# Performance work log

Measured on AMD Instinct MI355X. Metric: run time of the kernel, lower is better.

Reference implementation:

```python
import jax, jax.numpy as jnp
import numpy as np

ALPHA = 0.001  # plasticity learning rate from the source module
B, I, H = 64, 512, 1024
D = I + H


def _xavier(k, shape):
    fan_out, fan_in = shape
    lim = float(np.sqrt(6.0 / (fan_in + fan_out)))
    return jax.random.uniform(k, shape, minval=-lim, maxval=lim, dtype=jnp.float32)


def setup_inputs() -> dict:
    key = jax.random.key(0)
    ks = jax.random.split(key, 9)
    inputs = jax.random.normal(ks[0], (B, I), dtype=jnp.float32)
    hidden = 0.1 * jax.random.normal(ks[1], (B, H), dtype=jnp.float32)
    # per-sample plastic fast weights (nonzero to exercise the matvec path)
    wih = 0.01 * jax.random.normal(ks[2], (B, H, D), dtype=jnp.float32)
    Wih_a = _xavier(ks[3], (H, D))
    Wih_b = _xavier(ks[4], (H, D))
    Wih_c = _xavier(ks[5], (H, D))
    Wih_d = _xavier(ks[6], (H, D))
    bih = jnp.zeros((H,), dtype=jnp.float32)
    W_dop = _xavier(ks[7], (H, D))
    b_dop = jnp.zeros((H,), dtype=jnp.float32)
    return {"inputs": inputs, "hidden": hidden, "wih": wih,
            "Wih_a": Wih_a, "Wih_b": Wih_b, "Wih_c": Wih_c, "Wih_d": Wih_d,
            "bih": bih, "W_dop": W_dop, "b_dop": b_dop}


def reference(inputs, hidden, wih, Wih_a, Wih_b, Wih_c, Wih_d, bih, W_dop, b_dop):
    # x = cat(inputs, hidden): [B, D]
    x = jnp.concatenate([inputs, hidden], axis=1)
    # dopamine_signal is computed in the source but never used downstream;
    # kept here for fidelity (XLA will DCE it).
    _dopamine = jax.nn.sigmoid(x @ W_dop.T + b_dop)  # noqa: F841
    # batched matvec over the plastic fast weights: [B,H]
    new_hidden = jnp.tanh(jnp.einsum('bj,bkj->bk', x, wih) + bih)
    y = new_hidden[:, :, None]   # [B, H, 1]
    xb = x[:, None, :]           # [B, 1, D]
    # Hebbian outer-product update (the two 'ones' bmms are just broadcasts)
    wih_new = wih + ALPHA * (y * xb * Wih_a + xb * Wih_b + y * Wih_c + Wih_d)
    return new_hidden, wih_new
```

## Files before the change

kernel.cpp:

```cpp
#include <hip/hip_runtime.h>

constexpr int Bn = 64;
constexpr int In = 512;
constexpr int Hn = 1024;
constexpr int Dn = 1536;
constexpr float ALPHA = 0.001f;

typedef float nfloat4 __attribute__((ext_vector_type(4)));

__global__ __launch_bounds__(256) void prnn_fused_kernel(
    const float* __restrict__ inputs,
    const float* __restrict__ hidden,
    const float* __restrict__ wih,
    const float* __restrict__ Wa,
    const float* __restrict__ Wb,
    const float* __restrict__ Wc,
    const float* __restrict__ Wd,
    const float* __restrict__ bih,
    float* __restrict__ out_hidden,
    float* __restrict__ out_wih)
{
    __shared__ nfloat4 sW[4 * (Dn / 4)];

    const int k   = blockIdx.x;
    const int tid = threadIdx.x;

    {
        const nfloat4* wa4 = (const nfloat4*)(Wa + (size_t)k * Dn);
        const nfloat4* wb4 = (const nfloat4*)(Wb + (size_t)k * Dn);
        const nfloat4* wc4 = (const nfloat4*)(Wc + (size_t)k * Dn);
        const nfloat4* wd4 = (const nfloat4*)(Wd + (size_t)k * Dn);
        #pragma unroll
        for (int e = 0; e < 2; ++e) {
            const int i = tid + e * 256;
            if (i < 384) {
                sW[i]        = wa4[i] * ALPHA;
                sW[384 + i]  = wb4[i] * ALPHA;
                sW[768 + i]  = wc4[i] * ALPHA;
                sW[1152 + i] = wd4[i] * ALPHA;
            }
        }
    }
    __syncthreads();

    const int wave = tid >> 6;
    const int lane = tid & 63;
    const int b0   = wave * 16;
    const float bk = bih[k];
    const int base = lane * 4;

    nfloat4 w[4][6];
    nfloat4 xb[2][6];

    auto load_x = [&](int b, nfloat4 (&x)[6]) {
        const float* __restrict__ xin  = inputs + b * In;
        const float* __restrict__ xhid = hidden + b * Hn;
        #pragma unroll
        for (int c = 0; c < 6; ++c) {
            const int idx = c * 256 + base;
            x[c] = (c < 2) ? *(const nfloat4*)(xin + idx)
                           : *(const nfloat4*)(xhid + (idx - In));
        }
    };

    #pragma unroll
    for (int g = 0; g < 4; ++g) {
        const int bg = b0 + g * 4;

        #pragma unroll
        for (int q = 0; q < 4; ++q) {
            const float* __restrict__ wrow =
                wih + ((size_t)(bg + q) * Hn + k) * Dn;
            #pragma unroll
            for (int c = 0; c < 6; ++c)
                w[q][c] = *(const nfloat4*)(wrow + c * 256 + base);
        }
        load_x(bg, xb[0]);

        #pragma unroll
        for (int q = 0; q < 4; ++q) {
            if (q < 3) load_x(bg + q + 1, xb[(q + 1) & 1]);
            nfloat4 (&x)[6] = xb[q & 1];

            float acc = 0.0f;
            #pragma unroll
            for (int c = 0; c < 6; ++c) {
                nfloat4 p = w[q][c] * x[c];
                acc += (p.x + p.y) + (p.z + p.w);
            }
            #pragma unroll
            for (int off = 32; off > 0; off >>= 1)
                acc += __shfl_xor(acc, off, 64);

            const float y = tanhf(acc + bk);
            const int b = bg + q;
            if (lane == 0) out_hidden[b * Hn + k] = y;

            float* __restrict__ orow = out_wih + ((size_t)b * Hn + k) * Dn;
            #pragma unroll
            for (int c = 0; c < 6; ++c) {
                const int e = c * 64 + lane;
                const nfloat4 m1 = x[c] * sW[e]       + sW[768 + e];
                const nfloat4 m2 = x[c] * sW[384 + e] + sW[1152 + e];
                const nfloat4 o  = (w[q][c] + m2) + y * m1;
                __builtin_nontemporal_store(o, (nfloat4*)(orow + c * 256 + base));
            }
        }
    }
}

extern "C" void kernel_launch(void* const* d_in, const int* in_sizes, int n_in,
                              void* d_out, int out_size, void* d_ws, size_t ws_size,
                              hipStream_t stream) {
    const float* inputs = (const float*)d_in[0];
    const float* hidden = (const float*)d_in[1];
    const float* wih    = (const float*)d_in[2];
    const float* Wa     = (const float*)d_in[3];
    const float* Wb     = (const float*)d_in[4];
    const float* Wc     = (const float*)d_in[5];
    const float* Wd     = (const float*)d_in[6];
    const float* bih    = (const float*)d_in[7];

    float* out_hidden = (float*)d_out;
    float* out_wih    = (float*)d_out + (size_t)Bn * Hn;

    prnn_fused_kernel<<<dim3(Hn), dim3(256), 0, stream>>>(
        inputs, hidden, wih, Wa, Wb, Wc, Wd, bih, out_hidden, out_wih);
}
```

Before: 164.3 us.

## Remap blocks to (batch, 64-row k tile) and stream shared weights from L2

The work split changes from one block per hidden row k (covering all batches) to one block per (batch, 64-row chunk of k). Each wave handles 16 rows and keeps its x vector in registers for the whole block. The LDS staging of the four Wa..Wd rows is removed; those rows are now read straight from global memory for every (b,k), relying on L2/LLC reuse across the 64 batch blocks. The wih row loads are double-buffered so the next row is in flight during the current compute. In exchange, global read traffic for the shared weights rises unless the cache absorbs it.

```diff
diff --git a/kernel.cpp b/kernel.cpp
--- a/kernel.cpp
+++ b/kernel.cpp
@@ -20,91 +20,83 @@
     float* __restrict__ out_hidden,
     float* __restrict__ out_wih)
 {
-    __shared__ nfloat4 sW[4 * (Dn / 4)];
-
-    const int k   = blockIdx.x;
-    const int tid = threadIdx.x;
-
-    {
-        const nfloat4* wa4 = (const nfloat4*)(Wa + (size_t)k * Dn);
-        const nfloat4* wb4 = (const nfloat4*)(Wb + (size_t)k * Dn);
-        const nfloat4* wc4 = (const nfloat4*)(Wc + (size_t)k * Dn);
-        const nfloat4* wd4 = (const nfloat4*)(Wd + (size_t)k * Dn);
-        #pragma unroll
-        for (int e = 0; e < 2; ++e) {
-            const int i = tid + e * 256;
-            if (i < 384) {
-                sW[i]        = wa4[i] * ALPHA;
-                sW[384 + i]  = wb4[i] * ALPHA;
-                sW[768 + i]  = wc4[i] * ALPHA;
-                sW[1152 + i] = wd4[i] * ALPHA;
-            }
-        }
-    }
-    __syncthreads();
-
-    const int wave = tid >> 6;
-    const int lane = tid & 63;
-    const int b0   = wave * 16;
-    const float bk = bih[k];
+    const int bid  = blockIdx.x;
+    const int k0   = (bid & 15) << 6;
+    const int b    = bid >> 4;
+    const int wv   = threadIdx.x >> 6;
+    const int lane = threadIdx.x & 63;
     const int base = lane * 4;
 
-    nfloat4 w[4][6];
-    nfloat4 xb[2][6];
-
-    auto load_x = [&](int b, nfloat4 (&x)[6]) {
-        const float* __restrict__ xin  = inputs + b * In;
-        const float* __restrict__ xhid = hidden + b * Hn;
+    nfloat4 x[6];
+    {
+        const float* __restrict__ xin = inputs + b * In;
+        const float* __restrict__ xh  = hidden + b * Hn;
         #pragma unroll
         for (int c = 0; c < 6; ++c) {
             const int idx = c * 256 + base;
             x[c] = (c < 2) ? *(const nfloat4*)(xin + idx)
-                           : *(const nfloat4*)(xhid + (idx - In));
+                           : *(const nfloat4*)(xh + (idx - In));
         }
+    }
+
+    nfloat4 wb2[2][6];
+
+    auto wrow_ptr = [&](int i) {
+        const int k = k0 + wv + (i << 2);
+        return wih + ((size_t)b * Hn + k) * Dn;
     };
 
+    {
+        const float* __restrict__ p = wrow_ptr(0);
+        #pragma unroll
+        for (int c = 0; c < 6; ++c)
+            wb2[0][c] = *(const nfloat4*)(p + c * 256 + base);
+    }
+
     #pragma unroll
-    for (int g = 0; g < 4; ++g) {
-        const int bg = b0 + g * 4;
+    for (int i = 0; i < 16; ++i) {
+        const int k = k0 + wv + (i << 2);
+
+        if (i + 1 < 16) {
+            const float* __restrict__ p = wrow_ptr(i + 1);
+            #pragma unroll
+            for (int c = 0; c < 6; ++c)
+                wb2[(i + 1) & 1][c] = *(const nfloat4*)(p + c * 256 + base);
+        }
+        nfloat4 (&w)[6] = wb2[i & 1];
+
+        float acc = 0.0f;
+        #pragma unroll
+        for (int c = 0; c < 6; ++c) {
+            const nfloat4 p = w[c] * x[c];
+            acc += (p.x + p.y) + (p.z + p.w);
+        }
+        #pragma unroll
+        for (int off = 32; off > 0; off >>= 1)
+            acc += __shfl_xor(acc, off, 64);
+
+        const float y  = tanhf(acc + bih[k]);
+        const float ay = ALPHA * y;
+        if (lane == 0) out_hidden[b * Hn + k] = y;
+
+        const float* __restrict__ pa = Wa + (size_t)k * Dn;
+        const float* __restrict__ pb = Wb + (size_t)k * Dn;
+        const float* __restrict__ pc = Wc + (size_t)k * Dn;
+        const float* __restrict__ pd = Wd + (size_t)k * Dn;
+        float* __restrict__ orow = out_wih + ((size_t)b * Hn + k) * Dn;
 
         #pragma unroll
-        for (int q = 0; q < 4; ++q) {
-            const float* __restrict__ wrow =
-                wih + ((size_t)(bg + q) * Hn + k) * Dn;
-            #pragma unroll
-            for (int c = 0; c < 6; ++c)
-                w[q][c] = *(const nfloat4*)(wrow + c * 256 + base);
-        }
-        load_x(bg, xb[0]);
-
-        #pragma unroll
-        for (int q = 0; q < 4; ++q) {
-            if (q < 3) load_x(bg + q + 1, xb[(q + 1) & 1]);
-            nfloat4 (&x)[6] = xb[q & 1];
-
-            float acc = 0.0f;
-            #pragma unroll
-            for (int c = 0; c < 6; ++c) {
-                nfloat4 p = w[q][c] * x[c];
-                acc += (p.x + p.y) + (p.z + p.w);
-            }
-            #pragma unroll
-            for (int off = 32; off > 0; off >>= 1)
-                acc += __shfl_xor(acc, off, 64);
-
-            const float y = tanhf(acc + bk);
-            const int b = bg + q;
-            if (lane == 0) out_hidden[b * Hn + k] = y;
-
-            float* __restrict__ orow = out_wih + ((size_t)b * Hn + k) * Dn;
-            #pragma unroll
-            for (int c = 0; c < 6; ++c) {
-                const int e = c * 64 + lane;
-                const nfloat4 m1 = x[c] * sW[e]       + sW[768 + e];
-                const nfloat4 m2 = x[c] * sW[384 + e] + sW[1152 + e];
-                const nfloat4 o  = (w[q][c] + m2) + y * m1;
-                __builtin_nontemporal_store(o, (nfloat4*)(orow + c * 256 + base));
-            }
+        for (int c = 0; c < 6; ++c) {
+            const int idx = c * 256 + base;
+            const nfloat4 a4 = *(const nfloat4*)(pa + idx);
+            const nfloat4 b4 = *(const nfloat4*)(pb + idx);
+            const nfloat4 c4 = *(const nfloat4*)(pc + idx);
+            const nfloat4 d4 = *(const nfloat4*)(pd + idx);
+            const nfloat4 t1 = x[c] * a4 + c4;
+            const nfloat4 t2 = x[c] * b4 + d4;
+            nfloat4 o = w[c] + ALPHA * t2;
+            o = o + ay * t1;
+            __builtin_nontemporal_store(o, (nfloat4*)(orow + idx));
         }
     }
 }
@@ -124,6 +116,6 @@
     float* out_hidden = (float*)d_out;
     float* out_wih    = (float*)d_out + (size_t)Bn * Hn;
 
-    prnn_fused_kernel<<<dim3(Hn), dim3(256), 0, stream>>>(
+    prnn_fused_kernel<<<dim3(Bn * 16), dim3(256), 0, stream>>>(
         inputs, hidden, wih, Wa, Wb, Wc, Wd, bih, out_hidden, out_wih);
 }
```

Result: slower. 199.6 us (+21.5%).
